# Kernel tuning notes

Measured on AMD Instinct MI355X. Metric: run time of the kernel, lower is better.

Reference implementation:

```python
import jax, jax.numpy as jnp
import numpy as np

NUM_GROUP = 256   # scene-level NUM_GROUP == max_token_num
GROUP_SIZE = 64   # scene-level GROUP_SIZE
N_POINTS = 40000  # scene_npoints


def setup_inputs() -> dict:
    key = jax.random.key(0)
    k1, k2, k3 = jax.random.split(key, 3)
    B = 2
    xyzs = jax.random.uniform(k1, (B, N_POINTS, 3), jnp.float32)
    pointcloud_features = jax.random.normal(k2, (B, N_POINTS, 768), jnp.float32)
    valid_labels = jax.random.randint(k3, (B, N_POINTS), 0, 2, dtype=jnp.int32)
    return {"xyzs": xyzs, "pointcloud_features": pointcloud_features,
            "valid_labels": valid_labels}


def _fps(xyz, n_samples):
    # Farthest point sampling. xyz: [B,N,3] -> indices [B,G]
    B, N, _ = xyz.shape
    init_idx = jnp.zeros((B,), jnp.int32)          # start from point 0
    dist0 = jnp.full((B, N), 1e10, xyz.dtype)

    def step(carry, _):
        dist, last = carry
        p = jnp.take_along_axis(xyz, last[:, None, None], axis=1)   # [B,1,3]
        d = jnp.sum((xyz - p) ** 2, axis=-1)                        # [B,N]
        dist = jnp.minimum(dist, d)
        nxt = jnp.argmax(dist, axis=-1).astype(jnp.int32)
        return (dist, nxt), nxt

    (_, _), rest = jax.lax.scan(step, (dist0, init_idx), None, length=n_samples - 1)
    return jnp.concatenate([init_idx[None, :], rest], axis=0).T     # [B,G]


def _knn_idx(xyz, center, k):
    # squared distances [B,G,N], then k nearest point indices per center
    d = (jnp.sum(center ** 2, -1)[..., None]
         + jnp.sum(xyz ** 2, -1)[:, None, :]
         - 2.0 * jnp.einsum('bgc,bnc->bgn', center, xyz))
    _, idx = jax.lax.top_k(-d, k)
    return idx                                                      # [B,G,k]


def reference(xyzs, pointcloud_features, valid_labels):
    # All batch elements are 'scene' level; max_token_num == NUM_GROUP, so
    # the scatter-into-padded-tensor is the identity placement.
    B, _, dim = pointcloud_features.shape
    xyz = xyzs[:, :N_POINTS, :]
    fts = pointcloud_features[:, :N_POINTS, :]
    valid = valid_labels[:, :N_POINTS].astype(fts.dtype)
    points = jnp.concatenate([xyz, fts, valid[..., None]], axis=-1)  # [B,N,3+dim+1]

    fps_idx = _fps(xyz, NUM_GROUP)                                   # [B,G]
    scene_center = jnp.take_along_axis(xyz, fps_idx[..., None], axis=1)  # [B,G,3]
    knn = _knn_idx(xyz, scene_center, GROUP_SIZE)                    # [B,G,M]

    neighborhood = jax.vmap(lambda p, i: p[i])(points, knn)          # [B,G,M,C]
    # Group tokenizer recenters xyz channels around the group center
    neighborhood = neighborhood.at[..., :3].add(-scene_center[:, :, None, :])

    all_fts = neighborhood[..., 3:-1].mean(axis=-2)                  # [B,G,dim]
    all_fts_mask = (neighborhood[..., -1].sum(axis=-1) > 0).astype(fts.dtype)  # [B,G]
    return all_fts, all_fts_mask, scene_center
```

## Files before the change

### kernel.cpp

```cpp
#include <hip/hip_runtime.h>
#include <cstddef>

#define NPTS   40000
#define NGRP   256
#define GSZ    64
#define FDIM   768
#define BATCH  2

#define FPS_BPB    32
#define FPS_NBLK   (FPS_BPB * BATCH)
#define FPS_TPB    64
#define FPS_PPB    (NPTS / FPS_BPB)
#define FPS_PPT    20
#define MB_ROUNDS  255
#define NCHUNK     (NPTS / 64)

__device__ __forceinline__ unsigned long long mk32(float v, unsigned tb) {
    return ((unsigned long long)__float_as_uint(v) << 16) | (unsigned long long)tb;
}
__device__ __forceinline__ float d2f(float px, float py, float pz,
                                     float cx, float cy, float cz) {
    float dx = __fsub_rn(px, cx), dy = __fsub_rn(py, cy), dz = __fsub_rn(pz, cz);
    return __fmaf_rn(dz, dz, __fmaf_rn(dy, dy, __fmul_rn(dx, dx)));
}
__device__ __forceinline__ unsigned long long knn_key(double v, int idx) {
    unsigned long long bits = (unsigned long long)__double_as_longlong(v);
    return (bits & 0xFFFFFFFFFFFF0000ull) | (unsigned long long)(unsigned)idx;
}
__device__ __forceinline__ unsigned long long fps_mk64(double v, unsigned tb) {
    return (((unsigned long long)__double_as_longlong(v)) & 0xFFFFFFFFFFFF0000ull)
         | (unsigned long long)tb;
}
__device__ __forceinline__ unsigned long long wave_max_u64(unsigned long long k) {
#pragma unroll
    for (int off = 32; off >= 1; off >>= 1) {
        unsigned long long o = __shfl_xor(k, off, 64);
        k = o > k ? o : k;
    }
    return k;
}

#define LANE_RESCAN(OUT)                                                    \
    {                                                                       \
        unsigned long long bb_ = 0ull;                                      \
        _Pragma("unroll")                                                   \
        for (int j_ = 0; j_ < FPS_PPT; ++j_) {                              \
            bool live_ = (((vmask >> j_) & 1u) != 0u) &&                    \
                         (((cons >> j_) & 1u) == 0u);                       \
            unsigned long long kk_ = live_                                  \
                ? mk32(dist[j_], tb0 - (unsigned)(j_ << 6)) : 0ull;         \
            bb_ = kk_ > bb_ ? kk_ : bb_;                                    \
        }                                                                   \
        OUT = bb_;                                                          \
    }

template<int M>
__global__ void __launch_bounds__(FPS_TPB) fps_spec_kernel(
    const float* __restrict__ xyz,
    float* __restrict__ centers,
    unsigned long long* __restrict__ mb)
{
    constexpr int Q     = (FPS_BPB * M) / 64;
    constexpr int MB_RW = FPS_NBLK * M;

    const int bid  = blockIdx.x;
    const int b    = bid >> 5;
    const int lb   = bid & 31;
    const int lane = threadIdx.x;
    const float* __restrict__ X = xyz + (size_t)b * NPTS * 3;
    const int base = lb * FPS_PPB;
    const unsigned tb0 = 0xFFFFu - (unsigned)(base + lane);

    float px[FPS_PPT], py[FPS_PPT], pz[FPS_PPT], dist[FPS_PPT];
    unsigned vmask = 0;
#pragma unroll
    for (int j = 0; j < FPS_PPT; ++j) {
        int loc = lane + j * FPS_TPB;
        bool ok = loc < FPS_PPB;
        int i   = base + (ok ? loc : 0);
        px[j] = X[i * 3 + 0]; py[j] = X[i * 3 + 1]; pz[j] = X[i * 3 + 2];
        if (ok) vmask |= 1u << j;
    }

    {
        float cx = X[0], cy = X[1], cz = X[2];
        if (lb == 0 && lane == 0) {
            centers[(size_t)(b * NGRP) * 3 + 0] = cx;
            centers[(size_t)(b * NGRP) * 3 + 1] = cy;
            centers[(size_t)(b * NGRP) * 3 + 2] = cz;
        }
#pragma unroll
        for (int j = 0; j < FPS_PPT; ++j)
            dist[j] = d2f(px[j], py[j], pz[j], cx, cy, cz);
    }

    int done = 1;
    int r = 0;

    while (done < NGRP) {
        unsigned long long s0 = 0, s1 = 0, s2 = 0, s3 = 0;
#pragma unroll
        for (int j = 0; j < FPS_PPT; ++j) {
            bool live = ((vmask >> j) & 1u) != 0u;
            unsigned long long kk = live ? mk32(dist[j], tb0 - (unsigned)(j << 6)) : 0ull;
            unsigned long long t;
            t = kk > s0 ? kk : s0;  kk = kk > s0 ? s0 : kk;  s0 = t;
            t = kk > s1 ? kk : s1;  kk = kk > s1 ? s1 : kk;  s1 = t;
            t = kk > s2 ? kk : s2;  kk = kk > s2 ? s2 : kk;  s2 = t;
            s3 = kk > s3 ? kk : s3;
        }
        unsigned cons = 0;

        unsigned long long myMsg = 0;
#pragma unroll
        for (int i = 0; i < M; ++i) {
            if (s0 == 0ull) LANE_RESCAN(s0);
            unsigned long long g = wave_max_u64(s0);
            if (s0 == g && g != 0ull) {
                unsigned idx = 0xFFFFu - (unsigned)(g & 0xFFFFull);
                unsigned jj  = (idx - (unsigned)(base + lane)) >> 6;
                cons |= 1u << jj;
                s0 = s1; s1 = s2; s2 = s3; s3 = 0ull;
            }
            myMsg = (lane == i) ? g : myMsg;
        }

        if (lane < M)
            __hip_atomic_store(&mb[(size_t)r * MB_RW + bid * M + lane], myMsg,
                               __ATOMIC_RELAXED, __HIP_MEMORY_SCOPE_AGENT);

        const unsigned long long* pb = mb + (size_t)r * MB_RW + b * (FPS_BPB * M);
        unsigned long long w[Q];
#pragma unroll
        for (int q = 0; q < Q; ++q)
            w[q] = __hip_atomic_load(pb + lane + 64 * q,
                                     __ATOMIC_RELAXED, __HIP_MEMORY_SCOPE_AGENT);
        for (;;) {
            bool miss = false;
#pragma unroll
            for (int q = 0; q < Q; ++q) miss |= (w[q] == 0ull);
            if (__ballot(miss) == 0ull) break;
#pragma unroll
            for (int q = 0; q < Q; ++q)
                if (w[q] == 0ull)
                    w[q] = __hip_atomic_load(pb + lane + 64 * q,
                                             __ATOMIC_RELAXED, __HIP_MEMORY_SCOPE_AGENT);
        }

        unsigned long long tl = 0;
        if ((lane & (M - 1)) == (M - 1)) {
#pragma unroll
            for (int q = 0; q < Q; ++q) tl = w[q] > tl ? w[q] : tl;
        }
        const unsigned long long T = wave_max_u64(tl);

        float cvv[Q]; unsigned ctb[Q]; unsigned long long ck[Q];
        float ccx[Q], ccy[Q], ccz[Q];
#pragma unroll
        for (int q = 0; q < Q; ++q) {
            ck[q]  = w[q];
            ctb[q] = (unsigned)(w[q] & 0xFFFFull);
            cvv[q] = __uint_as_float((unsigned)(w[q] >> 16));
            int ii = (int)(0xFFFFu - ctb[q]);
            ccx[q] = X[ii * 3 + 0]; ccy[q] = X[ii * 3 + 1]; ccz[q] = X[ii * 3 + 2];
        }
        unsigned consq = 0;

#pragma unroll 1
        for (int s = 0; s < 64; ++s) {
            unsigned long long lk = 0;
#pragma unroll
            for (int q = 0; q < Q; ++q) {
                unsigned long long kk = ((consq >> q) & 1u) ? 0ull : ck[q];
                lk = kk > lk ? kk : lk;
            }
            unsigned long long g = wave_max_u64(lk);
            if (s > 0 && g < T) break;

            float sx = ccx[0], sy = ccy[0], sz = ccz[0];
#pragma unroll
            for (int q = 0; q < Q; ++q) {
                bool hit = (ck[q] == g) && !((consq >> q) & 1u);
                consq |= hit ? (1u << q) : 0u;
                sx = hit ? ccx[q] : sx;
                sy = hit ? ccy[q] : sy;
                sz = hit ? ccz[q] : sz;
            }
            unsigned long long om = __ballot(lk == g);
            int owner = __ffsll((long long)om) - 1;
            float wx = __shfl(sx, owner, 64);
            float wy = __shfl(sy, owner, 64);
            float wz = __shfl(sz, owner, 64);
            if (lb == 0 && lane == 0) {
                centers[((size_t)b * NGRP + done) * 3 + 0] = wx;
                centers[((size_t)b * NGRP + done) * 3 + 1] = wy;
                centers[((size_t)b * NGRP + done) * 3 + 2] = wz;
            }
#pragma unroll
            for (int q = 0; q < Q; ++q) {
                cvv[q] = fminf(cvv[q], d2f(ccx[q], ccy[q], ccz[q], wx, wy, wz));
                ck[q]  = ((consq >> q) & 1u) ? 0ull
                       : (((unsigned long long)__float_as_uint(cvv[q]) << 16)
                          | (unsigned long long)ctb[q]);
            }
#pragma unroll
            for (int j = 0; j < FPS_PPT; ++j)
                dist[j] = fminf(dist[j], d2f(px[j], py[j], pz[j], wx, wy, wz));
            ++done;
            if (done == NGRP) break;
        }
        ++r;
    }
}

__global__ void __launch_bounds__(FPS_TPB) fps_kernel(
    const float* __restrict__ xyz,
    float* __restrict__ centers,
    unsigned long long* __restrict__ keys)
{
    const int bid  = blockIdx.x;
    const int b    = bid >> 5;
    const int lb   = bid & 31;
    const int lane = threadIdx.x;
    const float* __restrict__ X = xyz + (size_t)b * NPTS * 3;
    const int base  = lb * FPS_PPB;
    const int gbase = base + lane;

    double px[FPS_PPT], py[FPS_PPT], pz[FPS_PPT], dist[FPS_PPT];
#pragma unroll
    for (int j = 0; j < FPS_PPT; ++j) {
        int loc = lane + j * FPS_TPB;
        bool ok = loc < FPS_PPB;
        int i   = base + (ok ? loc : 0);
        px[j] = (double)X[i * 3 + 0];
        py[j] = (double)X[i * 3 + 1];
        pz[j] = (double)X[i * 3 + 2];
        dist[j] = ok ? 1e18 : -1.0;
    }
    double cx = (double)X[0], cy = (double)X[1], cz = (double)X[2];
    if (lb == 0 && lane == 0) {
        centers[(size_t)(b * NGRP) * 3 + 0] = X[0];
        centers[(size_t)(b * NGRP) * 3 + 1] = X[1];
        centers[(size_t)(b * NGRP) * 3 + 2] = X[2];
    }
    for (int it = 0; it < NGRP - 1; ++it) {
        double bd = -2.0; int bj = 0;
#pragma unroll
        for (int j = 0; j < FPS_PPT; ++j) {
            double dx = px[j] - cx, dy = py[j] - cy, dz = pz[j] - cz;
            double d  = fma(dz, dz, fma(dy, dy, dx * dx));
            double nd = dist[j] < d ? dist[j] : d;
            dist[j] = nd;
            bool better = nd > bd;
            bd = better ? nd : bd;
            bj = better ? j  : bj;
        }
        unsigned long long key = fps_mk64(bd, 0xFFFFu - (unsigned)(gbase + (bj << 6)));
        key = wave_max_u64(key);
        if (lane == 0)
            __hip_atomic_store(&keys[it * FPS_NBLK + bid], key,
                               __ATOMIC_RELAXED, __HIP_MEMORY_SCOPE_AGENT);
        unsigned long long pk = 0;
        if (lane < FPS_BPB) {
            const unsigned long long* sp = &keys[it * FPS_NBLK + b * FPS_BPB + lane];
            do {
                pk = __hip_atomic_load(sp, __ATOMIC_RELAXED, __HIP_MEMORY_SCOPE_AGENT);
            } while (pk == 0ull);
        }
        unsigned long long g = wave_max_u64(pk);
        int widx = 0xFFFF - (int)(g & 0xFFFFull);
        float wx = X[widx * 3 + 0], wy = X[widx * 3 + 1], wz = X[widx * 3 + 2];
        cx = (double)wx; cy = (double)wy; cz = (double)wz;
        if (lb == 0 && lane == 0) {
            centers[(size_t)(b * NGRP + it + 1) * 3 + 0] = wx;
            centers[(size_t)(b * NGRP + it + 1) * 3 + 1] = wy;
            centers[(size_t)(b * NGRP + it + 1) * 3 + 2] = wz;
        }
    }
}

__global__ void __launch_bounds__(256) knn_agg_kernel(
    const float* __restrict__ xyz,
    const float* __restrict__ fts,
    const int*   __restrict__ valid,
    const float* __restrict__ centers,
    float* __restrict__ all_fts,
    float* __restrict__ mask)
{
    const int c    = blockIdx.x;
    const int b    = c >> 8;
    const int tid  = threadIdx.x;
    const int wid  = tid >> 6;
    const int lane = tid & 63;
    const float* __restrict__ X = xyz + (size_t)b * NPTS * 3;

    const double cx = (double)centers[(size_t)c * 3 + 0];
    const double cy = (double)centers[(size_t)c * 3 + 1];
    const double cz = (double)centers[(size_t)c * 3 + 2];

    unsigned long long slot;
    {
        int i = wid * 64 + lane;
        float x = X[i * 3 + 0], y = X[i * 3 + 1], z = X[i * 3 + 2];
        double dx = (double)x - cx, dy = (double)y - cy, dz = (double)z - cz;
        slot = knn_key(dx * dx + dy * dy + dz * dz, i);
    }
    unsigned long long tau = wave_max_u64(slot);

    float ax, ay, az, bx, by, bz;
    {
        int ia = (wid + 4) * 64 + lane;
        ax = X[ia * 3 + 0]; ay = X[ia * 3 + 1]; az = X[ia * 3 + 2];
        int sb = wid + 8 < NCHUNK ? wid + 8 : NCHUNK - 1;
        int ib = sb * 64 + lane;
        bx = X[ib * 3 + 0]; by = X[ib * 3 + 1]; bz = X[ib * 3 + 2];
    }
    for (int s = wid + 4; s < NCHUNK; s += 4) {
        float x = ax, y = ay, z = az;
        ax = bx; ay = by; az = bz;
        int sp = s + 8 < NCHUNK ? s + 8 : NCHUNK - 1;
        int ip = sp * 64 + lane;
        bx = X[ip * 3 + 0]; by = X[ip * 3 + 1]; bz = X[ip * 3 + 2];

        int i = s * 64 + lane;
        double dx = (double)x - cx, dy = (double)y - cy, dz = (double)z - cz;
        unsigned long long key = knn_key(dx * dx + dy * dy + dz * dz, i);

        unsigned long long cand = __ballot(key < tau);
        while (cand) {
            int l = __ffsll(cand) - 1;
            cand &= cand - 1;
            unsigned long long kc = __shfl(key, l, 64);
            if (kc < tau) {
                unsigned long long om = __ballot(slot == tau);
                int owner = __ffsll(om) - 1;
                if (lane == owner) slot = kc;
                tau = wave_max_u64(slot);
            }
        }
    }

    __shared__ unsigned long long skey[256];
    __shared__ int s_nbr[GSZ];
    skey[tid] = slot;
    __syncthreads();
#pragma unroll
    for (int k = 2; k <= 256; k <<= 1) {
        for (int j = k >> 1; j > 0; j >>= 1) {
            int ixj = tid ^ j;
            if (ixj > tid) {
                unsigned long long a = skey[tid], bb = skey[ixj];
                bool up = ((tid & k) == 0);
                if ((a > bb) == up) { skey[tid] = bb; skey[ixj] = a; }
            }
            __syncthreads();
        }
    }

    if (wid == 0) {
        int idx = (int)(skey[lane] & 0xFFFFull);
        s_nbr[lane] = idx;
        int v = valid[b * NPTS + idx];
        unsigned long long vb = __ballot(v != 0);
        if (lane == 0) mask[c] = vb ? 1.0f : 0.0f;
    }
    __syncthreads();

    const float* __restrict__ F = fts + (size_t)b * NPTS * FDIM;
    float a0 = 0.f, a1 = 0.f, a2 = 0.f, b0 = 0.f, b1 = 0.f, b2 = 0.f;
#pragma unroll 1
    for (int j = 0; j < GSZ; j += 2) {
        const float* r0 = F + (size_t)s_nbr[j]     * FDIM;
        const float* r1 = F + (size_t)s_nbr[j + 1] * FDIM;
        a0 += r0[tid];       b0 += r1[tid];
        a1 += r0[tid + 256]; b1 += r1[tid + 256];
        a2 += r0[tid + 512]; b2 += r1[tid + 512];
    }
    float* o = all_fts + (size_t)c * FDIM;
    o[tid]       = (a0 + b0) * 0.015625f;
    o[tid + 256] = (a1 + b1) * 0.015625f;
    o[tid + 512] = (a2 + b2) * 0.015625f;
}

extern "C" void kernel_launch(void* const* d_in, const int* in_sizes, int n_in,
                              void* d_out, int out_size, void* d_ws, size_t ws_size,
                              hipStream_t stream) {
    const float* xyz   = (const float*)d_in[0];
    const float* fts   = (const float*)d_in[1];
    const int*   valid = (const int*)d_in[2];

    float* out     = (float*)d_out;
    float* all_fts = out;
    float* mask    = out + (size_t)BATCH * NGRP * FDIM;
    float* centers = mask + (size_t)BATCH * NGRP;

    const size_t mb16 = (size_t)MB_ROUNDS * FPS_NBLK * 16 * 8;
    unsigned long long* mb = (unsigned long long*)d_ws;

    if (ws_size >= mb16) {
        hipMemsetAsync(d_ws, 0, mb16, stream);
        fps_spec_kernel<16><<<dim3(FPS_NBLK), dim3(FPS_TPB), 0, stream>>>(xyz, centers, mb);
    } else {
        hipMemsetAsync(d_ws, 0, (size_t)MB_ROUNDS * FPS_NBLK * 8, stream);
        fps_kernel<<<dim3(FPS_NBLK), dim3(FPS_TPB), 0, stream>>>(xyz, centers, mb);
    }

    knn_agg_kernel<<<dim3(BATCH * NGRP), dim3(256), 0, stream>>>(
        xyz, fts, valid, centers, all_fts, mask);
}
```

Measured before the change: 602.0 us.

## Use speculative per-lane top-4 selection with bitonic sort in FPS and KNN

In FPS, each wave now bitonic-sorts all lanes' top-4 candidates across registers with shuffles to pick the top M in one pass. It falls back to the old serial M-round wave-max extraction only when a lane's fourth candidate could rank in the top M. In KNN, each thread keeps a private top-4 over a strided scan, the block bitonic-sorts 1024 candidates in shared memory, and the old ballot-driven insertion scan runs only when some thread's fourth key beats the 64th overall. This replaces data-dependent serial reductions with fixed sorting networks, at the cost of extra sort work and a possible slow fallback path.

```diff
diff --git a/kernel.cpp b/kernel.cpp
--- a/kernel.cpp
+++ b/kernel.cpp
@@ -81,7 +81,6 @@
         px[j] = X[i * 3 + 0]; py[j] = X[i * 3 + 1]; pz[j] = X[i * 3 + 2];
         if (ok) vmask |= 1u << j;
     }
-
     {
         float cx = X[0], cy = X[1], cz = X[2];
         if (lb == 0 && lane == 0) {
@@ -109,20 +108,59 @@
             t = kk > s2 ? kk : s2;  kk = kk > s2 ? s2 : kk;  s2 = t;
             s3 = kk > s3 ? kk : s3;
         }
-        unsigned cons = 0;
-
-        unsigned long long myMsg = 0;
-#pragma unroll
-        for (int i = 0; i < M; ++i) {
-            if (s0 == 0ull) LANE_RESCAN(s0);
-            unsigned long long g = wave_max_u64(s0);
-            if (s0 == g && g != 0ull) {
-                unsigned idx = 0xFFFFu - (unsigned)(g & 0xFFFFull);
-                unsigned jj  = (idx - (unsigned)(base + lane)) >> 6;
-                cons |= 1u << jj;
-                s0 = s1; s1 = s2; s2 = s3; s3 = 0ull;
-            }
-            myMsg = (lane == i) ? g : myMsg;
+
+        unsigned long long v[4] = { s0, s1, s2, s3 };
+#pragma unroll
+        for (int k = 2; k <= 256; k <<= 1) {
+#pragma unroll
+            for (int j = k >> 1; j > 0; j >>= 1) {
+                if (j >= 64) {
+                    const int jr = j >> 6;
+#pragma unroll
+                    for (int rr = 0; rr < 4; ++rr) {
+                        const int pr = rr ^ jr;
+                        if (pr > rr) {
+                            const bool desc = (((rr << 6) & k) == 0);
+                            unsigned long long a = v[rr], bb2 = v[pr];
+                            unsigned long long mx = a > bb2 ? a : bb2;
+                            unsigned long long mn = a > bb2 ? bb2 : a;
+                            v[rr] = desc ? mx : mn;
+                            v[pr] = desc ? mn : mx;
+                        }
+                    }
+                } else {
+#pragma unroll
+                    for (int rr = 0; rr < 4; ++rr) {
+                        unsigned long long o = __shfl_xor(v[rr], j, 64);
+                        const bool lower = ((lane & j) == 0);
+                        const bool desc  = (((lane + (rr << 6)) & k) == 0);
+                        const bool takeMax = (lower == desc);
+                        unsigned long long mx = v[rr] > o ? v[rr] : o;
+                        unsigned long long mn = v[rr] > o ? o : v[rr];
+                        v[rr] = takeMax ? mx : mn;
+                    }
+                }
+            }
+        }
+        unsigned long long k16 = __shfl(v[0], 15, 64);
+        bool fail = (__ballot(s3 > k16) != 0ull);
+
+        unsigned long long myMsg = (lane < M) ? v[0] : 0ull;
+        if (fail) {
+            unsigned cons = 0;
+            myMsg = 0;
+#pragma unroll
+            for (int i = 0; i < M; ++i) {
+                if (s0 == 0ull) LANE_RESCAN(s0);
+                unsigned long long g = wave_max_u64(s0);
+                if (s0 == g && g != 0ull) {
+                    unsigned idx = 0xFFFFu - (unsigned)(g & 0xFFFFull);
+                    unsigned jj  = (idx - (unsigned)(base + lane)) >> 6;
+                    cons |= 1u << jj;
+                    s0 = s1; s1 = s2; s2 = s3; s3 = 0ull;
+                }
+                myMsg = (lane == i) ? g : myMsg;
+            }
         }
 
         if (lane < M)
@@ -294,75 +332,109 @@
     const int lane = tid & 63;
     const float* __restrict__ X = xyz + (size_t)b * NPTS * 3;
 
+    __shared__ unsigned long long skey[1024];
+    __shared__ int s_nbr[GSZ];
+    __shared__ int s_fail;
+
     const double cx = (double)centers[(size_t)c * 3 + 0];
     const double cy = (double)centers[(size_t)c * 3 + 1];
     const double cz = (double)centers[(size_t)c * 3 + 2];
 
-    unsigned long long slot;
+    unsigned long long m0 = ~0ull, m1 = ~0ull, m2 = ~0ull, m3 = ~0ull;
+#pragma unroll 2
+    for (int s = 0; s < 157; ++s) {
+        int i = s * 256 + tid;
+        if (i < NPTS) {
+            float x = X[i * 3 + 0], y = X[i * 3 + 1], z = X[i * 3 + 2];
+            double dx = (double)x - cx, dy = (double)y - cy, dz = (double)z - cz;
+            unsigned long long key = knn_key(dx * dx + dy * dy + dz * dz, i);
+            if (key < m3) {
+                unsigned long long t;
+                t = key < m0 ? m0 : key;  m0 = key < m0 ? key : m0;  key = t;
+                t = key < m1 ? m1 : key;  m1 = key < m1 ? key : m1;  key = t;
+                t = key < m2 ? m2 : key;  m2 = key < m2 ? key : m2;  key = t;
+                m3 = key < m3 ? key : m3;
+            }
+        }
+    }
+    skey[tid]       = m0;
+    skey[tid + 256] = m1;
+    skey[tid + 512] = m2;
+    skey[tid + 768] = m3;
+    if (tid == 0) s_fail = 0;
+    __syncthreads();
+
+    for (int k = 2; k <= 1024; k <<= 1) {
+        for (int j = k >> 1; j > 0; j >>= 1) {
+#pragma unroll
+            for (int rr = 0; rr < 4; ++rr) {
+                int idx = tid + 256 * rr;
+                int ixj = idx ^ j;
+                if (ixj > idx) {
+                    unsigned long long a = skey[idx], bb2 = skey[ixj];
+                    bool up = ((idx & k) == 0);
+                    if ((a > bb2) == up) { skey[idx] = bb2; skey[ixj] = a; }
+                }
+            }
+            __syncthreads();
+        }
+    }
     {
-        int i = wid * 64 + lane;
-        float x = X[i * 3 + 0], y = X[i * 3 + 1], z = X[i * 3 + 2];
-        double dx = (double)x - cx, dy = (double)y - cy, dz = (double)z - cz;
-        slot = knn_key(dx * dx + dy * dy + dz * dz, i);
-    }
-    unsigned long long tau = wave_max_u64(slot);
-
-    float ax, ay, az, bx, by, bz;
-    {
-        int ia = (wid + 4) * 64 + lane;
-        ax = X[ia * 3 + 0]; ay = X[ia * 3 + 1]; az = X[ia * 3 + 2];
-        int sb = wid + 8 < NCHUNK ? wid + 8 : NCHUNK - 1;
-        int ib = sb * 64 + lane;
-        bx = X[ib * 3 + 0]; by = X[ib * 3 + 1]; bz = X[ib * 3 + 2];
-    }
-    for (int s = wid + 4; s < NCHUNK; s += 4) {
-        float x = ax, y = ay, z = az;
-        ax = bx; ay = by; az = bz;
-        int sp = s + 8 < NCHUNK ? s + 8 : NCHUNK - 1;
-        int ip = sp * 64 + lane;
-        bx = X[ip * 3 + 0]; by = X[ip * 3 + 1]; bz = X[ip * 3 + 2];
-
-        int i = s * 64 + lane;
-        double dx = (double)x - cx, dy = (double)y - cy, dz = (double)z - cz;
-        unsigned long long key = knn_key(dx * dx + dy * dy + dz * dz, i);
-
-        unsigned long long cand = __ballot(key < tau);
-        while (cand) {
-            int l = __ffsll(cand) - 1;
-            cand &= cand - 1;
-            unsigned long long kc = __shfl(key, l, 64);
-            if (kc < tau) {
-                unsigned long long om = __ballot(slot == tau);
-                int owner = __ffsll(om) - 1;
-                if (lane == owner) slot = kc;
-                tau = wave_max_u64(slot);
-            }
-        }
-    }
-
-    __shared__ unsigned long long skey[256];
-    __shared__ int s_nbr[GSZ];
-    skey[tid] = slot;
-    __syncthreads();
-#pragma unroll
-    for (int k = 2; k <= 256; k <<= 1) {
-        for (int j = k >> 1; j > 0; j >>= 1) {
-            int ixj = tid ^ j;
-            if (ixj > tid) {
-                unsigned long long a = skey[tid], bb = skey[ixj];
-                bool up = ((tid & k) == 0);
-                if ((a > bb) == up) { skey[tid] = bb; skey[ixj] = a; }
-            }
-            __syncthreads();
-        }
-    }
-
-    if (wid == 0) {
-        int idx = (int)(skey[lane] & 0xFFFFull);
-        s_nbr[lane] = idx;
+        unsigned long long t64 = skey[63];
+        if (m3 < t64) s_fail = 1;
+        __syncthreads();
+    }
+
+    if (s_fail) {
+        __syncthreads();
+        unsigned long long slot;
+        {
+            int i = wid * 64 + lane;
+            float x = X[i * 3 + 0], y = X[i * 3 + 1], z = X[i * 3 + 2];
+            double dx = (double)x - cx, dy = (double)y - cy, dz = (double)z - cz;
+            slot = knn_key(dx * dx + dy * dy + dz * dz, i);
+        }
+        unsigned long long tau = wave_max_u64(slot);
+        for (int s = wid + 4; s < NCHUNK; s += 4) {
+            int i = s * 64 + lane;
+            float x = X[i * 3 + 0], y = X[i * 3 + 1], z = X[i * 3 + 2];
+            double dx = (double)x - cx, dy = (double)y - cy, dz = (double)z - cz;
+            unsigned long long key = knn_key(dx * dx + dy * dy + dz * dz, i);
+            unsigned long long cand = __ballot(key < tau);
+            while (cand) {
+                int l = __ffsll(cand) - 1;
+                cand &= cand - 1;
+                unsigned long long kc = __shfl(key, l, 64);
+                if (kc < tau) {
+                    unsigned long long om = __ballot(slot == tau);
+                    int owner = __ffsll(om) - 1;
+                    if (lane == owner) slot = kc;
+                    tau = wave_max_u64(slot);
+                }
+            }
+        }
+        skey[tid] = slot;
+        __syncthreads();
+#pragma unroll
+        for (int k = 2; k <= 256; k <<= 1) {
+            for (int j = k >> 1; j > 0; j >>= 1) {
+                int ixj = tid ^ j;
+                if (ixj > tid) {
+                    unsigned long long a = skey[tid], bb2 = skey[ixj];
+                    bool up = ((tid & k) == 0);
+                    if ((a > bb2) == up) { skey[tid] = bb2; skey[ixj] = a; }
+                }
+                __syncthreads();
+            }
+        }
+    }
+
+    if (tid < GSZ) {
+        int idx = (int)(skey[tid] & 0xFFFFull);
+        s_nbr[tid] = idx;
         int v = valid[b * NPTS + idx];
         unsigned long long vb = __ballot(v != 0);
-        if (lane == 0) mask[c] = vb ? 1.0f : 0.0f;
+        if (tid == 0) mask[c] = vb ? 1.0f : 0.0f;
     }
     __syncthreads();
 
```

After: 711.6 us. 1.18x slower.

## Fuse FPS and kNN aggregation into one kernel with progress-counter overlap

Applied to the files above, without the earlier changes.

Merges the FPS blocks and the kNN/feature-aggregation blocks into a single launch. FPS blocks publish a per-batch count of finished centers through an atomic counter, and aggregation blocks spin-wait until their own center is available. This lets kNN and gather work overlap the long serial FPS instead of running after it. The risks are forward-progress deadlock if aggregation blocks occupy the CUs before the FPS blocks are resident, wasted wavefront slots from 256-thread FPS blocks that use only 64 threads, and polling traffic that could slow the FPS critical path.

```diff
diff --git a/kernel.cpp b/kernel.cpp
--- a/kernel.cpp
+++ b/kernel.cpp
@@ -14,6 +14,9 @@
 #define FPS_PPT    20
 #define MB_ROUNDS  255
 #define NCHUNK     (NPTS / 64)
+
+#define W_NBLK     (BATCH * NGRP)
+#define GRID_BLK   (FPS_NBLK + W_NBLK)
 
 __device__ __forceinline__ unsigned long long mk32(float v, unsigned tb) {
     return ((unsigned long long)__float_as_uint(v) << 16) | (unsigned long long)tb;
@@ -55,162 +58,278 @@
     }
 
 template<int M>
-__global__ void __launch_bounds__(FPS_TPB) fps_spec_kernel(
+__global__ void __launch_bounds__(256) fused_kernel(
     const float* __restrict__ xyz,
+    const float* __restrict__ fts,
+    const int*   __restrict__ valid,
+    float* __restrict__ all_fts,
+    float* __restrict__ mask,
     float* __restrict__ centers,
-    unsigned long long* __restrict__ mb)
+    unsigned long long* __restrict__ mb,
+    unsigned int* __restrict__ dcnt)
 {
     constexpr int Q     = (FPS_BPB * M) / 64;
     constexpr int MB_RW = FPS_NBLK * M;
 
-    const int bid  = blockIdx.x;
-    const int b    = bid >> 5;
-    const int lb   = bid & 31;
-    const int lane = threadIdx.x;
+    const int bid = blockIdx.x;
+    const int tid = threadIdx.x;
+
+    if (bid < FPS_NBLK) {
+        if (tid >= 64) return;
+        const int lane = tid;
+        const int b    = bid >> 5;
+        const int lb   = bid & 31;
+        const float* __restrict__ X = xyz + (size_t)b * NPTS * 3;
+        const int base = lb * FPS_PPB;
+        const unsigned tb0 = 0xFFFFu - (unsigned)(base + lane);
+
+        float px[FPS_PPT], py[FPS_PPT], pz[FPS_PPT], dist[FPS_PPT];
+        unsigned vmask = 0;
+#pragma unroll
+        for (int j = 0; j < FPS_PPT; ++j) {
+            int loc = lane + j * FPS_TPB;
+            bool ok = loc < FPS_PPB;
+            int i   = base + (ok ? loc : 0);
+            px[j] = X[i * 3 + 0]; py[j] = X[i * 3 + 1]; pz[j] = X[i * 3 + 2];
+            if (ok) vmask |= 1u << j;
+        }
+        {
+            float cx = X[0], cy = X[1], cz = X[2];
+            if (lb == 0 && lane == 0) {
+                centers[(size_t)(b * NGRP) * 3 + 0] = cx;
+                centers[(size_t)(b * NGRP) * 3 + 1] = cy;
+                centers[(size_t)(b * NGRP) * 3 + 2] = cz;
+                __hip_atomic_store(&dcnt[b], 1u,
+                                   __ATOMIC_RELEASE, __HIP_MEMORY_SCOPE_AGENT);
+            }
+#pragma unroll
+            for (int j = 0; j < FPS_PPT; ++j)
+                dist[j] = d2f(px[j], py[j], pz[j], cx, cy, cz);
+        }
+
+        int done = 1;
+        int r = 0;
+
+        while (done < NGRP) {
+            unsigned long long s0 = 0, s1 = 0, s2 = 0, s3 = 0;
+#pragma unroll
+            for (int j = 0; j < FPS_PPT; ++j) {
+                bool live = ((vmask >> j) & 1u) != 0u;
+                unsigned long long kk = live ? mk32(dist[j], tb0 - (unsigned)(j << 6)) : 0ull;
+                unsigned long long t;
+                t = kk > s0 ? kk : s0;  kk = kk > s0 ? s0 : kk;  s0 = t;
+                t = kk > s1 ? kk : s1;  kk = kk > s1 ? s1 : kk;  s1 = t;
+                t = kk > s2 ? kk : s2;  kk = kk > s2 ? s2 : kk;  s2 = t;
+                s3 = kk > s3 ? kk : s3;
+            }
+            unsigned cons = 0;
+
+            unsigned long long myMsg = 0;
+#pragma unroll
+            for (int i = 0; i < M; ++i) {
+                if (s0 == 0ull) LANE_RESCAN(s0);
+                unsigned long long g = wave_max_u64(s0);
+                if (s0 == g && g != 0ull) {
+                    unsigned idx = 0xFFFFu - (unsigned)(g & 0xFFFFull);
+                    unsigned jj  = (idx - (unsigned)(base + lane)) >> 6;
+                    cons |= 1u << jj;
+                    s0 = s1; s1 = s2; s2 = s3; s3 = 0ull;
+                }
+                myMsg = (lane == i) ? g : myMsg;
+            }
+
+            if (lane < M)
+                __hip_atomic_store(&mb[(size_t)r * MB_RW + bid * M + lane], myMsg,
+                                   __ATOMIC_RELAXED, __HIP_MEMORY_SCOPE_AGENT);
+
+            const unsigned long long* pb = mb + (size_t)r * MB_RW + b * (FPS_BPB * M);
+            unsigned long long w[Q];
+#pragma unroll
+            for (int q = 0; q < Q; ++q)
+                w[q] = __hip_atomic_load(pb + lane + 64 * q,
+                                         __ATOMIC_RELAXED, __HIP_MEMORY_SCOPE_AGENT);
+            for (;;) {
+                bool miss = false;
+#pragma unroll
+                for (int q = 0; q < Q; ++q) miss |= (w[q] == 0ull);
+                if (__ballot(miss) == 0ull) break;
+#pragma unroll
+                for (int q = 0; q < Q; ++q)
+                    if (w[q] == 0ull)
+                        w[q] = __hip_atomic_load(pb + lane + 64 * q,
+                                                 __ATOMIC_RELAXED, __HIP_MEMORY_SCOPE_AGENT);
+            }
+
+            unsigned long long tl = 0;
+            if ((lane & (M - 1)) == (M - 1)) {
+#pragma unroll
+                for (int q = 0; q < Q; ++q) tl = w[q] > tl ? w[q] : tl;
+            }
+            const unsigned long long T = wave_max_u64(tl);
+
+            float cvv[Q]; unsigned ctb[Q]; unsigned long long ck[Q];
+            float ccx[Q], ccy[Q], ccz[Q];
+#pragma unroll
+            for (int q = 0; q < Q; ++q) {
+                ck[q]  = w[q];
+                ctb[q] = (unsigned)(w[q] & 0xFFFFull);
+                cvv[q] = __uint_as_float((unsigned)(w[q] >> 16));
+                int ii = (int)(0xFFFFu - ctb[q]);
+                ccx[q] = X[ii * 3 + 0]; ccy[q] = X[ii * 3 + 1]; ccz[q] = X[ii * 3 + 2];
+            }
+            unsigned consq = 0;
+
+#pragma unroll 1
+            for (int s = 0; s < 64; ++s) {
+                unsigned long long lk = 0;
+#pragma unroll
+                for (int q = 0; q < Q; ++q) {
+                    unsigned long long kk = ((consq >> q) & 1u) ? 0ull : ck[q];
+                    lk = kk > lk ? kk : lk;
+                }
+                unsigned long long g = wave_max_u64(lk);
+                if (s > 0 && g < T) break;
+
+                float sx = ccx[0], sy = ccy[0], sz = ccz[0];
+#pragma unroll
+                for (int q = 0; q < Q; ++q) {
+                    bool hit = (ck[q] == g) && !((consq >> q) & 1u);
+                    consq |= hit ? (1u << q) : 0u;
+                    sx = hit ? ccx[q] : sx;
+                    sy = hit ? ccy[q] : sy;
+                    sz = hit ? ccz[q] : sz;
+                }
+                unsigned long long om = __ballot(lk == g);
+                int owner = __ffsll((long long)om) - 1;
+                float wx = __shfl(sx, owner, 64);
+                float wy = __shfl(sy, owner, 64);
+                float wz = __shfl(sz, owner, 64);
+                if (lb == 0 && lane == 0) {
+                    centers[((size_t)b * NGRP + done) * 3 + 0] = wx;
+                    centers[((size_t)b * NGRP + done) * 3 + 1] = wy;
+                    centers[((size_t)b * NGRP + done) * 3 + 2] = wz;
+                }
+#pragma unroll
+                for (int q = 0; q < Q; ++q) {
+                    cvv[q] = fminf(cvv[q], d2f(ccx[q], ccy[q], ccz[q], wx, wy, wz));
+                    ck[q]  = ((consq >> q) & 1u) ? 0ull
+                           : (((unsigned long long)__float_as_uint(cvv[q]) << 16)
+                              | (unsigned long long)ctb[q]);
+                }
+#pragma unroll
+                for (int j = 0; j < FPS_PPT; ++j)
+                    dist[j] = fminf(dist[j], d2f(px[j], py[j], pz[j], wx, wy, wz));
+                ++done;
+                if (done == NGRP) break;
+            }
+            if (lb == 0 && lane == 0)
+                __hip_atomic_store(&dcnt[b], (unsigned)done,
+                                   __ATOMIC_RELEASE, __HIP_MEMORY_SCOPE_AGENT);
+            ++r;
+        }
+        return;
+    }
+
+    const int w   = bid - FPS_NBLK;
+    const int c   = (w >> 1) + ((w & 1) << 8);
+    const int b   = c >> 8;
+    const int wid  = tid >> 6;
+    const int lane = tid & 63;
     const float* __restrict__ X = xyz + (size_t)b * NPTS * 3;
-    const int base = lb * FPS_PPB;
-    const unsigned tb0 = 0xFFFFu - (unsigned)(base + lane);
-
-    float px[FPS_PPT], py[FPS_PPT], pz[FPS_PPT], dist[FPS_PPT];
-    unsigned vmask = 0;
-#pragma unroll
-    for (int j = 0; j < FPS_PPT; ++j) {
-        int loc = lane + j * FPS_TPB;
-        bool ok = loc < FPS_PPB;
-        int i   = base + (ok ? loc : 0);
-        px[j] = X[i * 3 + 0]; py[j] = X[i * 3 + 1]; pz[j] = X[i * 3 + 2];
-        if (ok) vmask |= 1u << j;
-    }
 
     {
-        float cx = X[0], cy = X[1], cz = X[2];
-        if (lb == 0 && lane == 0) {
-            centers[(size_t)(b * NGRP) * 3 + 0] = cx;
-            centers[(size_t)(b * NGRP) * 3 + 1] = cy;
-            centers[(size_t)(b * NGRP) * 3 + 2] = cz;
-        }
-#pragma unroll
-        for (int j = 0; j < FPS_PPT; ++j)
-            dist[j] = d2f(px[j], py[j], pz[j], cx, cy, cz);
-    }
-
-    int done = 1;
-    int r = 0;
-
-    while (done < NGRP) {
-        unsigned long long s0 = 0, s1 = 0, s2 = 0, s3 = 0;
-#pragma unroll
-        for (int j = 0; j < FPS_PPT; ++j) {
-            bool live = ((vmask >> j) & 1u) != 0u;
-            unsigned long long kk = live ? mk32(dist[j], tb0 - (unsigned)(j << 6)) : 0ull;
-            unsigned long long t;
-            t = kk > s0 ? kk : s0;  kk = kk > s0 ? s0 : kk;  s0 = t;
-            t = kk > s1 ? kk : s1;  kk = kk > s1 ? s1 : kk;  s1 = t;
-            t = kk > s2 ? kk : s2;  kk = kk > s2 ? s2 : kk;  s2 = t;
-            s3 = kk > s3 ? kk : s3;
-        }
-        unsigned cons = 0;
-
-        unsigned long long myMsg = 0;
-#pragma unroll
-        for (int i = 0; i < M; ++i) {
-            if (s0 == 0ull) LANE_RESCAN(s0);
-            unsigned long long g = wave_max_u64(s0);
-            if (s0 == g && g != 0ull) {
-                unsigned idx = 0xFFFFu - (unsigned)(g & 0xFFFFull);
-                unsigned jj  = (idx - (unsigned)(base + lane)) >> 6;
-                cons |= 1u << jj;
-                s0 = s1; s1 = s2; s2 = s3; s3 = 0ull;
-            }
-            myMsg = (lane == i) ? g : myMsg;
-        }
-
-        if (lane < M)
-            __hip_atomic_store(&mb[(size_t)r * MB_RW + bid * M + lane], myMsg,
-                               __ATOMIC_RELAXED, __HIP_MEMORY_SCOPE_AGENT);
-
-        const unsigned long long* pb = mb + (size_t)r * MB_RW + b * (FPS_BPB * M);
-        unsigned long long w[Q];
-#pragma unroll
-        for (int q = 0; q < Q; ++q)
-            w[q] = __hip_atomic_load(pb + lane + 64 * q,
-                                     __ATOMIC_RELAXED, __HIP_MEMORY_SCOPE_AGENT);
-        for (;;) {
-            bool miss = false;
-#pragma unroll
-            for (int q = 0; q < Q; ++q) miss |= (w[q] == 0ull);
-            if (__ballot(miss) == 0ull) break;
-#pragma unroll
-            for (int q = 0; q < Q; ++q)
-                if (w[q] == 0ull)
-                    w[q] = __hip_atomic_load(pb + lane + 64 * q,
-                                             __ATOMIC_RELAXED, __HIP_MEMORY_SCOPE_AGENT);
-        }
-
-        unsigned long long tl = 0;
-        if ((lane & (M - 1)) == (M - 1)) {
-#pragma unroll
-            for (int q = 0; q < Q; ++q) tl = w[q] > tl ? w[q] : tl;
-        }
-        const unsigned long long T = wave_max_u64(tl);
-
-        float cvv[Q]; unsigned ctb[Q]; unsigned long long ck[Q];
-        float ccx[Q], ccy[Q], ccz[Q];
-#pragma unroll
-        for (int q = 0; q < Q; ++q) {
-            ck[q]  = w[q];
-            ctb[q] = (unsigned)(w[q] & 0xFFFFull);
-            cvv[q] = __uint_as_float((unsigned)(w[q] >> 16));
-            int ii = (int)(0xFFFFu - ctb[q]);
-            ccx[q] = X[ii * 3 + 0]; ccy[q] = X[ii * 3 + 1]; ccz[q] = X[ii * 3 + 2];
-        }
-        unsigned consq = 0;
-
+        const unsigned int want = (unsigned)(c & (NGRP - 1)) + 1u;
+        while (__hip_atomic_load(&dcnt[b], __ATOMIC_RELAXED, __HIP_MEMORY_SCOPE_AGENT) < want)
+            __builtin_amdgcn_s_sleep(64);
+        __builtin_amdgcn_fence(__ATOMIC_ACQUIRE, "agent");
+    }
+
+    const double cx = (double)centers[(size_t)c * 3 + 0];
+    const double cy = (double)centers[(size_t)c * 3 + 1];
+    const double cz = (double)centers[(size_t)c * 3 + 2];
+
+    unsigned long long slot;
+    {
+        int i = wid * 64 + lane;
+        float x = X[i * 3 + 0], y = X[i * 3 + 1], z = X[i * 3 + 2];
+        double dx = (double)x - cx, dy = (double)y - cy, dz = (double)z - cz;
+        slot = knn_key(dx * dx + dy * dy + dz * dz, i);
+    }
+    unsigned long long tau = wave_max_u64(slot);
+
+    float ax, ay, az, bx, by, bz;
+    {
+        int ia = (wid + 4) * 64 + lane;
+        ax = X[ia * 3 + 0]; ay = X[ia * 3 + 1]; az = X[ia * 3 + 2];
+        int sb = wid + 8 < NCHUNK ? wid + 8 : NCHUNK - 1;
+        int ib = sb * 64 + lane;
+        bx = X[ib * 3 + 0]; by = X[ib * 3 + 1]; bz = X[ib * 3 + 2];
+    }
+    for (int s = wid + 4; s < NCHUNK; s += 4) {
+        float x = ax, y = ay, z = az;
+        ax = bx; ay = by; az = bz;
+        int sp = s + 8 < NCHUNK ? s + 8 : NCHUNK - 1;
+        int ip = sp * 64 + lane;
+        bx = X[ip * 3 + 0]; by = X[ip * 3 + 1]; bz = X[ip * 3 + 2];
+
+        int i = s * 64 + lane;
+        double dx = (double)x - cx, dy = (double)y - cy, dz = (double)z - cz;
+        unsigned long long key = knn_key(dx * dx + dy * dy + dz * dz, i);
+
+        unsigned long long cand = __ballot(key < tau);
+        while (cand) {
+            int l = __ffsll(cand) - 1;
+            cand &= cand - 1;
+            unsigned long long kc = __shfl(key, l, 64);
+            if (kc < tau) {
+                unsigned long long om = __ballot(slot == tau);
+                int owner = __ffsll(om) - 1;
+                if (lane == owner) slot = kc;
+                tau = wave_max_u64(slot);
+            }
+        }
+    }
+
+    __shared__ unsigned long long skey[256];
+    __shared__ int s_nbr[GSZ];
+    skey[tid] = slot;
+    __syncthreads();
+#pragma unroll
+    for (int k = 2; k <= 256; k <<= 1) {
+        for (int j = k >> 1; j > 0; j >>= 1) {
+            int ixj = tid ^ j;
+            if (ixj > tid) {
+                unsigned long long a = skey[tid], bb = skey[ixj];
+                bool up = ((tid & k) == 0);
+                if ((a > bb) == up) { skey[tid] = bb; skey[ixj] = a; }
+            }
+            __syncthreads();
+        }
+    }
+
+    if (wid == 0) {
+        int idx = (int)(skey[lane] & 0xFFFFull);
+        s_nbr[lane] = idx;
+        int v = valid[b * NPTS + idx];
+        unsigned long long vb = __ballot(v != 0);
+        if (lane == 0) mask[c] = vb ? 1.0f : 0.0f;
+    }
+    __syncthreads();
+
+    const float* __restrict__ F = fts + (size_t)b * NPTS * FDIM;
+    float a0 = 0.f, a1 = 0.f, a2 = 0.f, b0 = 0.f, b1 = 0.f, b2 = 0.f;
 #pragma unroll 1
-        for (int s = 0; s < 64; ++s) {
-            unsigned long long lk = 0;
-#pragma unroll
-            for (int q = 0; q < Q; ++q) {
-                unsigned long long kk = ((consq >> q) & 1u) ? 0ull : ck[q];
-                lk = kk > lk ? kk : lk;
-            }
-            unsigned long long g = wave_max_u64(lk);
-            if (s > 0 && g < T) break;
-
-            float sx = ccx[0], sy = ccy[0], sz = ccz[0];
-#pragma unroll
-            for (int q = 0; q < Q; ++q) {
-                bool hit = (ck[q] == g) && !((consq >> q) & 1u);
-                consq |= hit ? (1u << q) : 0u;
-                sx = hit ? ccx[q] : sx;
-                sy = hit ? ccy[q] : sy;
-                sz = hit ? ccz[q] : sz;
-            }
-            unsigned long long om = __ballot(lk == g);
-            int owner = __ffsll((long long)om) - 1;
-            float wx = __shfl(sx, owner, 64);
-            float wy = __shfl(sy, owner, 64);
-            float wz = __shfl(sz, owner, 64);
-            if (lb == 0 && lane == 0) {
-                centers[((size_t)b * NGRP + done) * 3 + 0] = wx;
-                centers[((size_t)b * NGRP + done) * 3 + 1] = wy;
-                centers[((size_t)b * NGRP + done) * 3 + 2] = wz;
-            }
-#pragma unroll
-            for (int q = 0; q < Q; ++q) {
-                cvv[q] = fminf(cvv[q], d2f(ccx[q], ccy[q], ccz[q], wx, wy, wz));
-                ck[q]  = ((consq >> q) & 1u) ? 0ull
-                       : (((unsigned long long)__float_as_uint(cvv[q]) << 16)
-                          | (unsigned long long)ctb[q]);
-            }
-#pragma unroll
-            for (int j = 0; j < FPS_PPT; ++j)
-                dist[j] = fminf(dist[j], d2f(px[j], py[j], pz[j], wx, wy, wz));
-            ++done;
-            if (done == NGRP) break;
-        }
-        ++r;
-    }
+    for (int j = 0; j < GSZ; j += 2) {
+        const float* r0 = F + (size_t)s_nbr[j]     * FDIM;
+        const float* r1 = F + (size_t)s_nbr[j + 1] * FDIM;
+        a0 += r0[tid];       b0 += r1[tid];
+        a1 += r0[tid + 256]; b1 += r1[tid + 256];
+        a2 += r0[tid + 512]; b2 += r1[tid + 512];
+    }
+    float* o = all_fts + (size_t)c * FDIM;
+    o[tid]       = (a0 + b0) * 0.015625f;
+    o[tid + 256] = (a1 + b1) * 0.015625f;
+    o[tid + 512] = (a2 + b2) * 0.015625f;
 }
 
 __global__ void __launch_bounds__(FPS_TPB) fps_kernel(
@@ -396,15 +515,16 @@
 
     const size_t mb16 = (size_t)MB_ROUNDS * FPS_NBLK * 16 * 8;
     unsigned long long* mb = (unsigned long long*)d_ws;
-
-    if (ws_size >= mb16) {
-        hipMemsetAsync(d_ws, 0, mb16, stream);
-        fps_spec_kernel<16><<<dim3(FPS_NBLK), dim3(FPS_TPB), 0, stream>>>(xyz, centers, mb);
+    unsigned int* dcnt = (unsigned int*)((char*)d_ws + mb16);
+
+    if (ws_size >= mb16 + 64) {
+        hipMemsetAsync(d_ws, 0, mb16 + 64, stream);
+        fused_kernel<16><<<dim3(GRID_BLK), dim3(256), 0, stream>>>(
+            xyz, fts, valid, all_fts, mask, centers, mb, dcnt);
     } else {
-        hipMemsetAsync(d_ws, 0, (size_t)MB_ROUNDS * FPS_NBLK * 8, stream);
+        hipMemsetAsync(d_ws, 0, 131072, stream);
         fps_kernel<<<dim3(FPS_NBLK), dim3(FPS_TPB), 0, stream>>>(xyz, centers, mb);
-    }
-
-    knn_agg_kernel<<<dim3(BATCH * NGRP), dim3(256), 0, stream>>>(
-        xyz, fts, valid, centers, all_fts, mask);
-}
+        knn_agg_kernel<<<dim3(BATCH * NGRP), dim3(256), 0, stream>>>(
+            xyz, fts, valid, centers, all_fts, mask);
+    }
+}
```

Result: faster. 588.2 us, median of 2 (-2.3%).
